# Kernel tuning notes

Measured on AMD Instinct MI355X. Metric: run time of the kernel, lower is better.

The kernel has to match this reference:

```python
import jax, jax.numpy as jnp
import numpy as np

TOPK = 2
GATE_THRESHOLD = 0.5
GATE_ALPHA = 0.1
EPS = 1e-8


def setup_inputs() -> dict:
    key = jax.random.key(0)
    x = jax.random.normal(key, (8192, 1024), dtype=jnp.float32)
    return {"x": x}


def reference(x):
    B, D = x.shape
    # F.normalize(p=2, eps): x / max(||x||, eps)
    norm = jnp.linalg.norm(x, axis=-1, keepdims=True)
    xn = x / jnp.maximum(norm, EPS)

    # pairwise dots; diagonal (self) masked to -1; NN search is no_grad
    dots = jax.lax.stop_gradient(xn @ xn.T)  # [B, B]
    diag = jnp.arange(B)
    dots = dots.at[diag, diag].set(-1.0)
    _, idx = jax.lax.top_k(dots, TOPK)  # [B, TOPK]

    nn_vecs = xn[idx]  # [B, TOPK, D]
    # torch PairwiseDistance(2, eps): ||x1 - x2 + eps||_2
    diff = xn[:, None, :] - nn_vecs + EPS
    distances = jnp.sqrt(jnp.sum(diff * diff, axis=-1)).reshape(-1)  # [B*TOPK]
    losses = -jnp.log(distances + EPS)

    # gate enabled since gate_threshold > 0
    alpha = max(GATE_ALPHA, 1e-6)
    gate = jax.nn.sigmoid((losses - GATE_THRESHOLD) / alpha)
    lg = losses * gate
    weighted_mean = lg.mean()
    gated_mean = lg.sum() / jnp.maximum(gate.sum(), 1.0)
    return 0.5 * weighted_mean + 0.5 * gated_mean
```

## Files before the change

### kernel.cpp

```cpp
#include <hip/hip_runtime.h>
#include <math.h>

#define NROWS 8192
#define DIM   1024
#define BT    256
#define NCHUNK 32
#define NTRI  528
#define NKT   16
#define BK    64

typedef __bf16 bf16x8 __attribute__((ext_vector_type(8)));
typedef float  f32x4  __attribute__((ext_vector_type(4)));

__device__ __forceinline__ unsigned short f2bf(float f) {
    unsigned int u = __float_as_uint(f);
    u = (u + 0x7FFFu + ((u >> 16) & 1u)) >> 16;
    return (unsigned short)u;
}

__device__ __forceinline__ void gld16(const void* g, void* l) {
    __builtin_amdgcn_global_load_lds(
        (__attribute__((address_space(1))) void*)g,
        (__attribute__((address_space(3))) void*)l,
        16, 0, 0);
}

template<int N>
__device__ __forceinline__ float dppror(float v) {
    return __int_as_float(__builtin_amdgcn_update_dpp(
        0, __float_as_int(v), 0x120 + N, 0xF, 0xF, false));
}

__device__ __forceinline__ void t2push(float& a1, float& a2, float v) {
    float hi = fmaxf(a1, v);
    float lo = fminf(a1, v);
    a1 = hi;
    a2 = fmaxf(a2, lo);
}

__device__ __forceinline__ void t2merge(float& a1, float& a2, float b1, float b2) {
    float hi = fmaxf(a1, b1);
    float lo = fminf(a1, b1);
    a1 = hi;
    a2 = fmaxf(fmaxf(a2, b2), lo);
}

__global__ __launch_bounds__(256) void knorm(const float* __restrict__ x,
                                             unsigned short* __restrict__ xn) {
    const int w = threadIdx.x >> 6, lane = threadIdx.x & 63;
    const int row = blockIdx.x * 4 + w;
    const float4* src = (const float4*)(x + (size_t)row * DIM);
    float4 v[4];
    float ss = 0.0f;
    #pragma unroll
    for (int i = 0; i < 4; i++) {
        v[i] = src[lane + 64 * i];
        ss += v[i].x * v[i].x + v[i].y * v[i].y + v[i].z * v[i].z + v[i].w * v[i].w;
    }
    #pragma unroll
    for (int d = 1; d < 64; d <<= 1) ss += __shfl_xor(ss, d);
    const float inv = 1.0f / fmaxf(sqrtf(ss), 1e-8f);
    unsigned short* dst = xn + (size_t)row * DIM;
    #pragma unroll
    for (int i = 0; i < 4; i++) {
        uint2 o;
        o.x = (unsigned)f2bf(v[i].x * inv) | ((unsigned)f2bf(v[i].y * inv) << 16);
        o.y = (unsigned)f2bf(v[i].z * inv) | ((unsigned)f2bf(v[i].w * inv) << 16);
        *(uint2*)(dst + (size_t)(lane + 64 * i) * 4) = o;
    }
}

__global__ __launch_bounds__(512, 2) void kgram(const unsigned short* __restrict__ xn,
                                                float2* __restrict__ top2) {
    __shared__ __align__(16) char smem[131072];
    float (*st2r)[256][2] = (float (*)[256][2])(smem);
    float (*st2c)[256][2] = (float (*)[256][2])(smem + 8192);

    const int t = threadIdx.x;
    const int lane = t & 63;
    const int w = t >> 6;
    const int wr = w >> 2, wc = w & 3;
    const int g = lane >> 4, c = lane & 15;
    const int cswz = (c >> 1) & 3;

    const int bid = (blockIdx.x & 7) * 66 + (blockIdx.x >> 3);
    int by = (int)((sqrtf(8.0f * (float)bid + 1.0f) - 1.0f) * 0.5f);
    while ((by + 1) * (by + 2) / 2 <= bid) by++;
    while (by * (by + 1) / 2 > bid) by--;
    const int bx = bid - by * (by + 1) / 2;
    const bool diagTile = (bx == by);

    const int q0 = t, q1 = 512 + t;
    const int r0 = q0 >> 2, c0 = (q0 & 3) ^ ((r0 >> 1) & 3);
    const int r1 = q1 >> 2, c1 = (q1 & 3) ^ ((r1 >> 1) & 3);
    const unsigned short* gA0p = xn + (size_t)(by * BT + r0) * DIM + c0 * 8;
    const unsigned short* gA1p = xn + (size_t)(by * BT + r1) * DIM + c1 * 8;
    const unsigned short* gB0p = xn + (size_t)(bx * BT + r0) * DIM + c0 * 8;
    const unsigned short* gB1p = xn + (size_t)(bx * BT + r1) * DIM + c1 * 8;

    const int aOff = (wr * 128 + c) * 64 + ((g ^ cswz) & 3) * 16;
    const int bOff = 65536 + (wc * 64 + c) * 64 + ((g ^ cswz) & 3) * 16;

    f32x4 acc[8][4];
    #pragma unroll
    for (int m = 0; m < 8; m++)
        #pragma unroll
        for (int n = 0; n < 4; n++) acc[m][n] = (f32x4)0.0f;

    bf16x8 aX0, aX1, aX2, aX3, aY0, aY1, aY2, aY3;
    bf16x8 bA0, bA1, bA2, bA3, bB0, bB1, bB2, bB3;

#define STG_A(BUF, H, KT) do {                                   \
        char* _d = smem + (BUF) * 32768 + (H) * 16384 + t * 16;  \
        gld16(gA0p + (KT) * 64 + (H) * 32, _d);                  \
        gld16(gA1p + (KT) * 64 + (H) * 32, _d + 8192);           \
    } while (0)
#define STG_B(BUF, H, KT) do {                                           \
        char* _d = smem + 65536 + (BUF) * 32768 + (H) * 16384 + t * 16;  \
        gld16(gB0p + (KT) * 64 + (H) * 32, _d);                          \
        gld16(gB1p + (KT) * 64 + (H) * 32, _d + 8192);                   \
    } while (0)
#define LDA4(D0, D1, D2, D3, BUF, H, MH) do {                                 \
        const char* _p = smem + (BUF) * 32768 + (H) * 16384 + (MH) * 4096 + aOff; \
        D0 = *(const bf16x8*)(_p);                                            \
        D1 = *(const bf16x8*)(_p + 1024);                                     \
        D2 = *(const bf16x8*)(_p + 2048);                                     \
        D3 = *(const bf16x8*)(_p + 3072);                                     \
    } while (0)
#define LDB4(D0, D1, D2, D3, BUF, H) do {                        \
        const char* _p = smem + (BUF) * 32768 + (H) * 16384 + bOff; \
        D0 = *(const bf16x8*)(_p);                               \
        D1 = *(const bf16x8*)(_p + 1024);                        \
        D2 = *(const bf16x8*)(_p + 2048);                        \
        D3 = *(const bf16x8*)(_p + 3072);                        \
    } while (0)
#define MF(a, b, cc) __builtin_amdgcn_mfma_f32_16x16x32_bf16(a, b, cc, 0, 0, 0)
#define MQUAD(MB, A0_, A1_, A2_, A3_, B0_, B1_, B2_, B3_) do {              \
        acc[(MB)+0][0]=MF(A0_,B0_,acc[(MB)+0][0]); acc[(MB)+0][1]=MF(A0_,B1_,acc[(MB)+0][1]); \
        acc[(MB)+0][2]=MF(A0_,B2_,acc[(MB)+0][2]); acc[(MB)+0][3]=MF(A0_,B3_,acc[(MB)+0][3]); \
        acc[(MB)+1][0]=MF(A1_,B0_,acc[(MB)+1][0]); acc[(MB)+1][1]=MF(A1_,B1_,acc[(MB)+1][1]); \
        acc[(MB)+1][2]=MF(A1_,B2_,acc[(MB)+1][2]); acc[(MB)+1][3]=MF(A1_,B3_,acc[(MB)+1][3]); \
        acc[(MB)+2][0]=MF(A2_,B0_,acc[(MB)+2][0]); acc[(MB)+2][1]=MF(A2_,B1_,acc[(MB)+2][1]); \
        acc[(MB)+2][2]=MF(A2_,B2_,acc[(MB)+2][2]); acc[(MB)+2][3]=MF(A2_,B3_,acc[(MB)+2][3]); \
        acc[(MB)+3][0]=MF(A3_,B0_,acc[(MB)+3][0]); acc[(MB)+3][1]=MF(A3_,B1_,acc[(MB)+3][1]); \
        acc[(MB)+3][2]=MF(A3_,B2_,acc[(MB)+3][2]); acc[(MB)+3][3]=MF(A3_,B3_,acc[(MB)+3][3]); \
    } while (0)
#define BAR1_LGKM                                          \
        __builtin_amdgcn_sched_barrier(0);                 \
        __builtin_amdgcn_s_barrier();                      \
        asm volatile("s_waitcnt lgkmcnt(0)" ::: "memory"); \
        __builtin_amdgcn_sched_barrier(0)
#define ENDPH                                              \
        __builtin_amdgcn_sched_barrier(0);                 \
        __builtin_amdgcn_s_barrier()
#define ENDPH_VM(N)                                        \
        __builtin_amdgcn_sched_barrier(0);                 \
        asm volatile("s_waitcnt vmcnt(" #N ")" ::: "memory"); \
        __builtin_amdgcn_s_barrier()

#define KTILE(J, BUF, S12, S34, VMA, VMB) do {                         \
                                                     \
        LDA4(aX0, aX1, aX2, aX3, BUF, 0, 0);                           \
        LDB4(bA0, bA1, bA2, bA3, BUF, 0);                              \
        if (S12) STG_A((BUF) ^ 1, 1, (J) + 1);                         \
        BAR1_LGKM;                                                     \
        __builtin_amdgcn_s_setprio(1);                                 \
        MQUAD(0, aX0, aX1, aX2, aX3, bA0, bA1, bA2, bA3);              \
        __builtin_amdgcn_s_setprio(0);                                 \
        ENDPH;                                                         \
                                                     \
        LDA4(aY0, aY1, aY2, aY3, BUF, 0, 1);                           \
        if (S12) STG_B((BUF) ^ 1, 1, (J) + 1);                         \
        BAR1_LGKM;                                                     \
        __builtin_amdgcn_s_setprio(1);                                 \
        MQUAD(4, aY0, aY1, aY2, aY3, bA0, bA1, bA2, bA3);              \
        __builtin_amdgcn_s_setprio(0);                                 \
        ENDPH_VM(VMA);                                                 \
                                                     \
        LDA4(aX0, aX1, aX2, aX3, BUF, 1, 0);                           \
        LDB4(bB0, bB1, bB2, bB3, BUF, 1);                              \
        if (S34) STG_A(BUF, 0, (J) + 2);                               \
        BAR1_LGKM;                                                     \
        __builtin_amdgcn_s_setprio(1);                                 \
        MQUAD(0, aX0, aX1, aX2, aX3, bB0, bB1, bB2, bB3);              \
        __builtin_amdgcn_s_setprio(0);                                 \
        ENDPH;                                                         \
                                                     \
        LDA4(aY0, aY1, aY2, aY3, BUF, 1, 1);                           \
        if (S34) STG_B(BUF, 0, (J) + 2);                               \
        BAR1_LGKM;                                                     \
        __builtin_amdgcn_s_setprio(1);                                 \
        MQUAD(4, aY0, aY1, aY2, aY3, bB0, bB1, bB2, bB3);              \
        __builtin_amdgcn_s_setprio(0);                                 \
        ENDPH_VM(VMB);                                                 \
    } while (0)

    STG_A(0, 0, 0); STG_B(0, 0, 0);
    STG_A(0, 1, 0); STG_B(0, 1, 0);
    STG_A(1, 0, 1); STG_B(1, 0, 1);
    __builtin_amdgcn_sched_barrier(0);
    asm volatile("s_waitcnt vmcnt(8)" ::: "memory");
    __builtin_amdgcn_s_barrier();
    __builtin_amdgcn_sched_barrier(0);

    #pragma unroll 1
    for (int jj = 0; jj < 7; ++jj) {
        const int j0 = jj * 2;
        KTILE(j0,     0, 1, 1, 8, 8);
        KTILE(j0 + 1, 1, 1, 1, 8, 8);
    }
    KTILE(14, 0, 1, 0, 8, 4);
    KTILE(15, 1, 0, 0, 0, 0);

#undef KTILE
#undef ENDPH_VM
#undef ENDPH
#undef BAR1_LGKM
#undef MQUAD
#undef MF
#undef LDB4
#undef LDA4
#undef STG_B
#undef STG_A

    #pragma unroll
    for (int m = 0; m < 8; m++) {
        #pragma unroll
        for (int rr = 0; rr < 4; rr++) {
            const int lrow = wr * 128 + m * 16 + g * 4 + rr;
            float a1 = -1e30f, a2 = -1e30f;
            #pragma unroll
            for (int n = 0; n < 4; n++) {
                float v = acc[m][n][rr];
                if (diagTile && (wc * 64 + n * 16 + c) == lrow) v = -2.0f;
                t2push(a1, a2, v);
            }
            { float b1 = dppror<1>(a1), b2 = dppror<1>(a2); t2merge(a1, a2, b1, b2); }
            { float b1 = dppror<2>(a1), b2 = dppror<2>(a2); t2merge(a1, a2, b1, b2); }
            { float b1 = dppror<4>(a1), b2 = dppror<4>(a2); t2merge(a1, a2, b1, b2); }
            { float b1 = dppror<8>(a1), b2 = dppror<8>(a2); t2merge(a1, a2, b1, b2); }
            if (c == 0) { st2r[wc][lrow][0] = a1; st2r[wc][lrow][1] = a2; }
        }
    }
    if (!diagTile) {
        #pragma unroll
        for (int n = 0; n < 4; n++) {
            const int lcol = wc * 64 + n * 16 + c;
            float a1 = -1e30f, a2 = -1e30f;
            #pragma unroll
            for (int m = 0; m < 8; m++)
                #pragma unroll
                for (int rr = 0; rr < 4; rr++)
                    t2push(a1, a2, acc[m][n][rr]);
            #pragma unroll
            for (int d = 16; d < 64; d <<= 1) {
                float b1 = __shfl_xor(a1, d);
                float b2 = __shfl_xor(a2, d);
                t2merge(a1, a2, b1, b2);
            }
            if (g == 0) { st2c[wr][lcol][0] = a1; st2c[wr][lcol][1] = a2; }
        }
    }
    __syncthreads();
    if (t < 256) {
        float a1 = st2r[0][t][0], a2 = st2r[0][t][1];
        t2merge(a1, a2, st2r[1][t][0], st2r[1][t][1]);
        t2merge(a1, a2, st2r[2][t][0], st2r[2][t][1]);
        t2merge(a1, a2, st2r[3][t][0], st2r[3][t][1]);
        top2[(size_t)(by * BT + t) * NCHUNK + bx] = make_float2(a1, a2);
    } else if (!diagTile) {
        const int tc = t - 256;
        float a1 = st2c[0][tc][0], a2 = st2c[0][tc][1];
        t2merge(a1, a2, st2c[1][tc][0], st2c[1][tc][1]);
        top2[(size_t)(bx * BT + tc) * NCHUNK + by] = make_float2(a1, a2);
    }
}

__global__ __launch_bounds__(256) void kloss(const float2* __restrict__ top2,
                                             float2* __restrict__ partials) {
    const int t = threadIdx.x;
    const int w = t >> 6, lane = t & 63;
    const int row = blockIdx.x * 4 + w;
    float a1 = -1e30f, a2 = -1e30f;
    if (lane < NCHUNK) {
        float2 q = top2[(size_t)row * NCHUNK + lane];
        a1 = q.x; a2 = q.y;
    }
    #pragma unroll
    for (int d = 1; d < 64; d <<= 1) {
        float b1 = __shfl_xor(a1, d);
        float b2 = __shfl_xor(a2, d);
        t2merge(a1, a2, b1, b2);
    }
    __shared__ float2 wsum[4];
    if (lane == 0) {
        float slg = 0.0f, sg = 0.0f;
        float vs[2] = {a1, a2};
        #pragma unroll
        for (int i = 0; i < 2; i++) {
            float dd = sqrtf(fmaxf(2.0f - 2.0f * vs[i], 0.0f));
            float loss = -logf(dd + 1e-8f);
            float gate = 1.0f / (1.0f + expf(-(loss - 0.5f) * 10.0f));
            slg += loss * gate;
            sg += gate;
        }
        wsum[w] = make_float2(slg, sg);
    }
    __syncthreads();
    if (t == 0) {
        float a = 0.0f, b = 0.0f;
        #pragma unroll
        for (int i = 0; i < 4; i++) { a += wsum[i].x; b += wsum[i].y; }
        partials[blockIdx.x] = make_float2(a, b);
    }
}

__global__ __launch_bounds__(256) void kfinal(const float2* __restrict__ partials,
                                              float* __restrict__ out) {
    const int t = threadIdx.x;
    float a = 0.0f, b = 0.0f;
    for (int i = t; i < 2048; i += 256) {
        float2 p = partials[i];
        a += p.x; b += p.y;
    }
    #pragma unroll
    for (int d = 1; d < 64; d <<= 1) {
        a += __shfl_xor(a, d);
        b += __shfl_xor(b, d);
    }
    __shared__ float2 ws4[4];
    if ((t & 63) == 0) ws4[t >> 6] = make_float2(a, b);
    __syncthreads();
    if (t == 0) {
        float A = 0.0f, Bb = 0.0f;
        #pragma unroll
        for (int i = 0; i < 4; i++) { A += ws4[i].x; Bb += ws4[i].y; }
        float wm = A / 16384.0f;
        float gm = A / fmaxf(Bb, 1.0f);
        out[0] = 0.5f * wm + 0.5f * gm;
    }
}

extern "C" void kernel_launch(void* const* d_in, const int* in_sizes, int n_in,
                              void* d_out, int out_size, void* d_ws, size_t ws_size,
                              hipStream_t stream) {
    const float* x = (const float*)d_in[0];
    unsigned short* xn = (unsigned short*)d_ws;
    float2* top2 = (float2*)((char*)d_ws + (size_t)16 * 1024 * 1024);
    float2* partials = (float2*)((char*)d_ws + (size_t)20 * 1024 * 1024);
    float* out = (float*)d_out;

    knorm<<<NROWS / 4, 256, 0, stream>>>(x, xn);
    kgram<<<NTRI, 512, 0, stream>>>(xn, top2);
    kloss<<<2048, 256, 0, stream>>>(top2, partials);
    kfinal<<<1, 256, 0, stream>>>(partials, out);
}
```

Baseline: 180.7 us.

## Split gram tiles into half-tile blocks with triple-buffered BK=32 pipeline and atomic final reduction

Each 256x256 upper-triangular tile is split into two 128x256 half-tiles. That gives 1056 blocks of 256 threads instead of 528 blocks of 512, which should balance work better across CUs. The K loop becomes a three-stage buffered pipeline with BK=32 over 32 steps. Column top-2 results are written straight to a 64-slot per-row table, and the separate final kernel is replaced by atomics plus a last-block-done counter in kloss. The cost is more redundant B-tile loads per block, more global writes, and float atomic ordering nondeterminism.

```diff
diff --git a/kernel.cpp b/kernel.cpp
--- a/kernel.cpp
+++ b/kernel.cpp
@@ -4,10 +4,11 @@
 #define NROWS 8192
 #define DIM   1024
 #define BT    256
-#define NCHUNK 32
+#define SLOTS 64
 #define NTRI  528
-#define NKT   16
-#define BK    64
+#define NBLK  1056
+#define NKT   32
+#define BK    32
 
 typedef __bf16 bf16x8 __attribute__((ext_vector_type(8)));
 typedef float  f32x4  __attribute__((ext_vector_type(4)));
@@ -46,7 +47,13 @@
 }
 
 __global__ __launch_bounds__(256) void knorm(const float* __restrict__ x,
-                                             unsigned short* __restrict__ xn) {
+                                             unsigned short* __restrict__ xn,
+                                             float* __restrict__ red) {
+    if (blockIdx.x == 0 && threadIdx.x == 0) {
+        red[0] = 0.0f;
+        red[1] = 0.0f;
+        ((unsigned int*)red)[2] = 0u;
+    }
     const int w = threadIdx.x >> 6, lane = threadIdx.x & 63;
     const int row = blockIdx.x * 4 + w;
     const float4* src = (const float4*)(x + (size_t)row * DIM);
@@ -70,36 +77,31 @@
     }
 }
 
-__global__ __launch_bounds__(512, 2) void kgram(const unsigned short* __restrict__ xn,
+__global__ __launch_bounds__(256, 2) void kgram(const unsigned short* __restrict__ xn,
                                                 float2* __restrict__ top2) {
-    __shared__ __align__(16) char smem[131072];
-    float (*st2r)[256][2] = (float (*)[256][2])(smem);
-    float (*st2c)[256][2] = (float (*)[256][2])(smem + 8192);
+    __shared__ __align__(16) char smem[73728];
+    float (*st2r)[128][2] = (float (*)[128][2])(smem);
 
     const int t = threadIdx.x;
     const int lane = t & 63;
     const int w = t >> 6;
-    const int wr = w >> 2, wc = w & 3;
     const int g = lane >> 4, c = lane & 15;
     const int cswz = (c >> 1) & 3;
 
-    const int bid = (blockIdx.x & 7) * 66 + (blockIdx.x >> 3);
-    int by = (int)((sqrtf(8.0f * (float)bid + 1.0f) - 1.0f) * 0.5f);
-    while ((by + 1) * (by + 2) / 2 <= bid) by++;
-    while (by * (by + 1) / 2 > bid) by--;
-    const int bx = bid - by * (by + 1) / 2;
+    const int bswz = (blockIdx.x & 7) * 132 + (blockIdx.x >> 3);
+    const int tix = bswz >> 1, hh = bswz & 1;
+    int by = (int)((sqrtf(8.0f * (float)tix + 1.0f) - 1.0f) * 0.5f);
+    while ((by + 1) * (by + 2) / 2 <= tix) by++;
+    while (by * (by + 1) / 2 > tix) by--;
+    const int bx = tix - by * (by + 1) / 2;
     const bool diagTile = (bx == by);
 
-    const int q0 = t, q1 = 512 + t;
-    const int r0 = q0 >> 2, c0 = (q0 & 3) ^ ((r0 >> 1) & 3);
-    const int r1 = q1 >> 2, c1 = (q1 & 3) ^ ((r1 >> 1) & 3);
-    const unsigned short* gA0p = xn + (size_t)(by * BT + r0) * DIM + c0 * 8;
-    const unsigned short* gA1p = xn + (size_t)(by * BT + r1) * DIM + c1 * 8;
+    const int r0 = t >> 2;
+    const int c0 = (t & 3) ^ ((r0 >> 1) & 3);
+    const unsigned short* gA0p = xn + (size_t)(by * BT + hh * 128 + r0) * DIM + c0 * 8;
     const unsigned short* gB0p = xn + (size_t)(bx * BT + r0) * DIM + c0 * 8;
-    const unsigned short* gB1p = xn + (size_t)(bx * BT + r1) * DIM + c1 * 8;
-
-    const int aOff = (wr * 128 + c) * 64 + ((g ^ cswz) & 3) * 16;
-    const int bOff = 65536 + (wc * 64 + c) * 64 + ((g ^ cswz) & 3) * 16;
+
+    const int aBase = c * 64 + ((g ^ cswz) & 3) * 16;
 
     f32x4 acc[8][4];
     #pragma unroll
@@ -107,43 +109,46 @@
         #pragma unroll
         for (int n = 0; n < 4; n++) acc[m][n] = (f32x4)0.0f;
 
-    bf16x8 aX0, aX1, aX2, aX3, aY0, aY1, aY2, aY3;
-    bf16x8 bA0, bA1, bA2, bA3, bB0, bB1, bB2, bB3;
-
-#define STG_A(BUF, H, KT) do {                                   \
-        char* _d = smem + (BUF) * 32768 + (H) * 16384 + t * 16;  \
-        gld16(gA0p + (KT) * 64 + (H) * 32, _d);                  \
-        gld16(gA1p + (KT) * 64 + (H) * 32, _d + 8192);           \
-    } while (0)
-#define STG_B(BUF, H, KT) do {                                           \
-        char* _d = smem + 65536 + (BUF) * 32768 + (H) * 16384 + t * 16;  \
-        gld16(gB0p + (KT) * 64 + (H) * 32, _d);                          \
-        gld16(gB1p + (KT) * 64 + (H) * 32, _d + 8192);                   \
-    } while (0)
-#define LDA4(D0, D1, D2, D3, BUF, H, MH) do {                                 \
-        const char* _p = smem + (BUF) * 32768 + (H) * 16384 + (MH) * 4096 + aOff; \
-        D0 = *(const bf16x8*)(_p);                                            \
-        D1 = *(const bf16x8*)(_p + 1024);                                     \
-        D2 = *(const bf16x8*)(_p + 2048);                                     \
-        D3 = *(const bf16x8*)(_p + 3072);                                     \
-    } while (0)
-#define LDB4(D0, D1, D2, D3, BUF, H) do {                        \
-        const char* _p = smem + (BUF) * 32768 + (H) * 16384 + bOff; \
-        D0 = *(const bf16x8*)(_p);                               \
-        D1 = *(const bf16x8*)(_p + 1024);                        \
-        D2 = *(const bf16x8*)(_p + 2048);                        \
-        D3 = *(const bf16x8*)(_p + 3072);                        \
+    bf16x8 aX0, aX1, aX2, aX3, aY0, aY1, aY2, aY3, bX0, bX1, bX2, bX3;
+
+#define STG_A(BUF, KT) do {                                  \
+        char* _d = smem + (BUF) * 24576 + t * 16;            \
+        const unsigned short* _s = gA0p + (KT) * BK;         \
+        gld16(_s, _d);                                       \
+        gld16(_s + 65536, _d + 4096);                        \
+    } while (0)
+#define STG_B(BUF, KT) do {                                  \
+        char* _d = smem + (BUF) * 24576 + 8192 + t * 16;     \
+        const unsigned short* _s = gB0p + (KT) * BK;         \
+        gld16(_s, _d);                                       \
+        gld16(_s + 65536,  _d + 4096);                       \
+        gld16(_s + 131072, _d + 8192);                       \
+        gld16(_s + 196608, _d + 12288);                      \
+    } while (0)
+#define LDA4(D0, D1, D2, D3, BUF, MH) do {                              \
+        const char* _p = smem + (BUF) * 24576 + (MH) * 4096 + aBase;    \
+        D0 = *(const bf16x8*)(_p);                                      \
+        D1 = *(const bf16x8*)(_p + 1024);                               \
+        D2 = *(const bf16x8*)(_p + 2048);                               \
+        D3 = *(const bf16x8*)(_p + 3072);                               \
+    } while (0)
+#define LDB4(D0, D1, D2, D3, BUF) do {                                  \
+        const char* _p = smem + (BUF) * 24576 + 8192 + w * 4096 + aBase; \
+        D0 = *(const bf16x8*)(_p);                                      \
+        D1 = *(const bf16x8*)(_p + 1024);                               \
+        D2 = *(const bf16x8*)(_p + 2048);                               \
+        D3 = *(const bf16x8*)(_p + 3072);                               \
     } while (0)
 #define MF(a, b, cc) __builtin_amdgcn_mfma_f32_16x16x32_bf16(a, b, cc, 0, 0, 0)
-#define MQUAD(MB, A0_, A1_, A2_, A3_, B0_, B1_, B2_, B3_) do {              \
-        acc[(MB)+0][0]=MF(A0_,B0_,acc[(MB)+0][0]); acc[(MB)+0][1]=MF(A0_,B1_,acc[(MB)+0][1]); \
-        acc[(MB)+0][2]=MF(A0_,B2_,acc[(MB)+0][2]); acc[(MB)+0][3]=MF(A0_,B3_,acc[(MB)+0][3]); \
-        acc[(MB)+1][0]=MF(A1_,B0_,acc[(MB)+1][0]); acc[(MB)+1][1]=MF(A1_,B1_,acc[(MB)+1][1]); \
-        acc[(MB)+1][2]=MF(A1_,B2_,acc[(MB)+1][2]); acc[(MB)+1][3]=MF(A1_,B3_,acc[(MB)+1][3]); \
-        acc[(MB)+2][0]=MF(A2_,B0_,acc[(MB)+2][0]); acc[(MB)+2][1]=MF(A2_,B1_,acc[(MB)+2][1]); \
-        acc[(MB)+2][2]=MF(A2_,B2_,acc[(MB)+2][2]); acc[(MB)+2][3]=MF(A2_,B3_,acc[(MB)+2][3]); \
-        acc[(MB)+3][0]=MF(A3_,B0_,acc[(MB)+3][0]); acc[(MB)+3][1]=MF(A3_,B1_,acc[(MB)+3][1]); \
-        acc[(MB)+3][2]=MF(A3_,B2_,acc[(MB)+3][2]); acc[(MB)+3][3]=MF(A3_,B3_,acc[(MB)+3][3]); \
+#define MQUAD(MB, A0_, A1_, A2_, A3_) do {                                                    \
+        acc[(MB)+0][0]=MF(A0_,bX0,acc[(MB)+0][0]); acc[(MB)+0][1]=MF(A0_,bX1,acc[(MB)+0][1]); \
+        acc[(MB)+0][2]=MF(A0_,bX2,acc[(MB)+0][2]); acc[(MB)+0][3]=MF(A0_,bX3,acc[(MB)+0][3]); \
+        acc[(MB)+1][0]=MF(A1_,bX0,acc[(MB)+1][0]); acc[(MB)+1][1]=MF(A1_,bX1,acc[(MB)+1][1]); \
+        acc[(MB)+1][2]=MF(A1_,bX2,acc[(MB)+1][2]); acc[(MB)+1][3]=MF(A1_,bX3,acc[(MB)+1][3]); \
+        acc[(MB)+2][0]=MF(A2_,bX0,acc[(MB)+2][0]); acc[(MB)+2][1]=MF(A2_,bX1,acc[(MB)+2][1]); \
+        acc[(MB)+2][2]=MF(A2_,bX2,acc[(MB)+2][2]); acc[(MB)+2][3]=MF(A2_,bX3,acc[(MB)+2][3]); \
+        acc[(MB)+3][0]=MF(A3_,bX0,acc[(MB)+3][0]); acc[(MB)+3][1]=MF(A3_,bX1,acc[(MB)+3][1]); \
+        acc[(MB)+3][2]=MF(A3_,bX2,acc[(MB)+3][2]); acc[(MB)+3][3]=MF(A3_,bX3,acc[(MB)+3][3]); \
     } while (0)
 #define BAR1_LGKM                                          \
         __builtin_amdgcn_sched_barrier(0);                 \
@@ -158,61 +163,42 @@
         asm volatile("s_waitcnt vmcnt(" #N ")" ::: "memory"); \
         __builtin_amdgcn_s_barrier()
 
-#define KTILE(J, BUF, S12, S34, VMA, VMB) do {                         \
-                                                     \
-        LDA4(aX0, aX1, aX2, aX3, BUF, 0, 0);                           \
-        LDB4(bA0, bA1, bA2, bA3, BUF, 0);                              \
-        if (S12) STG_A((BUF) ^ 1, 1, (J) + 1);                         \
-        BAR1_LGKM;                                                     \
-        __builtin_amdgcn_s_setprio(1);                                 \
-        MQUAD(0, aX0, aX1, aX2, aX3, bA0, bA1, bA2, bA3);              \
-        __builtin_amdgcn_s_setprio(0);                                 \
-        ENDPH;                                                         \
-                                                     \
-        LDA4(aY0, aY1, aY2, aY3, BUF, 0, 1);                           \
-        if (S12) STG_B((BUF) ^ 1, 1, (J) + 1);                         \
-        BAR1_LGKM;                                                     \
-        __builtin_amdgcn_s_setprio(1);                                 \
-        MQUAD(4, aY0, aY1, aY2, aY3, bA0, bA1, bA2, bA3);              \
-        __builtin_amdgcn_s_setprio(0);                                 \
-        ENDPH_VM(VMA);                                                 \
-                                                     \
-        LDA4(aX0, aX1, aX2, aX3, BUF, 1, 0);                           \
-        LDB4(bB0, bB1, bB2, bB3, BUF, 1);                              \
-        if (S34) STG_A(BUF, 0, (J) + 2);                               \
-        BAR1_LGKM;                                                     \
-        __builtin_amdgcn_s_setprio(1);                                 \
-        MQUAD(0, aX0, aX1, aX2, aX3, bB0, bB1, bB2, bB3);              \
-        __builtin_amdgcn_s_setprio(0);                                 \
-        ENDPH;                                                         \
-                                                     \
-        LDA4(aY0, aY1, aY2, aY3, BUF, 1, 1);                           \
-        if (S34) STG_B(BUF, 0, (J) + 2);                               \
-        BAR1_LGKM;                                                     \
-        __builtin_amdgcn_s_setprio(1);                                 \
-        MQUAD(4, aY0, aY1, aY2, aY3, bB0, bB1, bB2, bB3);              \
-        __builtin_amdgcn_s_setprio(0);                                 \
-        ENDPH_VM(VMB);                                                 \
-    } while (0)
-
-    STG_A(0, 0, 0); STG_B(0, 0, 0);
-    STG_A(0, 1, 0); STG_B(0, 1, 0);
-    STG_A(1, 0, 1); STG_B(1, 0, 1);
+#define KSTEP(J, BUF, SBUF, DOSTG, ENDM)            \
+    do {                                            \
+        LDA4(aX0, aX1, aX2, aX3, BUF, 0);           \
+        LDB4(bX0, bX1, bX2, bX3, BUF);              \
+        if (DOSTG) STG_A(SBUF, (J) + 2);            \
+        BAR1_LGKM;                                  \
+        __builtin_amdgcn_s_setprio(1);              \
+        MQUAD(0, aX0, aX1, aX2, aX3);               \
+        __builtin_amdgcn_s_setprio(0);              \
+        ENDPH;                                      \
+        LDA4(aY0, aY1, aY2, aY3, BUF, 1);           \
+        if (DOSTG) STG_B(SBUF, (J) + 2);            \
+        BAR1_LGKM;                                  \
+        __builtin_amdgcn_s_setprio(1);              \
+        MQUAD(4, aY0, aY1, aY2, aY3);               \
+        __builtin_amdgcn_s_setprio(0);              \
+        ENDM;                                       \
+    } while (0)
+
+    STG_A(0, 0); STG_B(0, 0);
+    STG_A(1, 1); STG_B(1, 1);
     __builtin_amdgcn_sched_barrier(0);
-    asm volatile("s_waitcnt vmcnt(8)" ::: "memory");
+    asm volatile("s_waitcnt vmcnt(6)" ::: "memory");
     __builtin_amdgcn_s_barrier();
     __builtin_amdgcn_sched_barrier(0);
 
     #pragma unroll 1
-    for (int jj = 0; jj < 7; ++jj) {
-        const int j0 = jj * 2;
-        KTILE(j0,     0, 1, 1, 8, 8);
-        KTILE(j0 + 1, 1, 1, 1, 8, 8);
-    }
-    KTILE(14, 0, 1, 0, 8, 4);
-    KTILE(15, 1, 0, 0, 0, 0);
-
-#undef KTILE
+    for (int jj = 0; jj < 10; ++jj) {
+        KSTEP(3 * jj + 0, 0, 2, 1, ENDPH_VM(6));
+        KSTEP(3 * jj + 1, 1, 0, 1, ENDPH_VM(6));
+        KSTEP(3 * jj + 2, 2, 1, 1, ENDPH_VM(6));
+    }
+    KSTEP(30, 0, 0, 0, ENDPH_VM(0));
+    KSTEP(31, 1, 0, 0, (void)0);
+
+#undef KSTEP
 #undef ENDPH_VM
 #undef ENDPH
 #undef BAR1_LGKM
@@ -227,25 +213,24 @@
     for (int m = 0; m < 8; m++) {
         #pragma unroll
         for (int rr = 0; rr < 4; rr++) {
-            const int lrow = wr * 128 + m * 16 + g * 4 + rr;
+            const int lrow = m * 16 + g * 4 + rr;
             float a1 = -1e30f, a2 = -1e30f;
             #pragma unroll
             for (int n = 0; n < 4; n++) {
                 float v = acc[m][n][rr];
-                if (diagTile && (wc * 64 + n * 16 + c) == lrow) v = -2.0f;
+                if (diagTile && (w * 64 + n * 16 + c) == hh * 128 + lrow) v = -2.0f;
                 t2push(a1, a2, v);
             }
             { float b1 = dppror<1>(a1), b2 = dppror<1>(a2); t2merge(a1, a2, b1, b2); }
             { float b1 = dppror<2>(a1), b2 = dppror<2>(a2); t2merge(a1, a2, b1, b2); }
             { float b1 = dppror<4>(a1), b2 = dppror<4>(a2); t2merge(a1, a2, b1, b2); }
             { float b1 = dppror<8>(a1), b2 = dppror<8>(a2); t2merge(a1, a2, b1, b2); }
-            if (c == 0) { st2r[wc][lrow][0] = a1; st2r[wc][lrow][1] = a2; }
+            if (c == 0) { st2r[w][lrow][0] = a1; st2r[w][lrow][1] = a2; }
         }
     }
     if (!diagTile) {
         #pragma unroll
         for (int n = 0; n < 4; n++) {
-            const int lcol = wc * 64 + n * 16 + c;
             float a1 = -1e30f, a2 = -1e30f;
             #pragma unroll
             for (int m = 0; m < 8; m++)
@@ -258,32 +243,32 @@
                 float b2 = __shfl_xor(a2, d);
                 t2merge(a1, a2, b1, b2);
             }
-            if (g == 0) { st2c[wr][lcol][0] = a1; st2c[wr][lcol][1] = a2; }
+            if (g == 0)
+                top2[(size_t)(bx * BT + w * 64 + n * 16 + c) * SLOTS + 2 * by + hh] =
+                    make_float2(a1, a2);
         }
     }
     __syncthreads();
-    if (t < 256) {
+    if (t < 128) {
         float a1 = st2r[0][t][0], a2 = st2r[0][t][1];
         t2merge(a1, a2, st2r[1][t][0], st2r[1][t][1]);
         t2merge(a1, a2, st2r[2][t][0], st2r[2][t][1]);
         t2merge(a1, a2, st2r[3][t][0], st2r[3][t][1]);
-        top2[(size_t)(by * BT + t) * NCHUNK + bx] = make_float2(a1, a2);
-    } else if (!diagTile) {
-        const int tc = t - 256;
-        float a1 = st2c[0][tc][0], a2 = st2c[0][tc][1];
-        t2merge(a1, a2, st2c[1][tc][0], st2c[1][tc][1]);
-        top2[(size_t)(bx * BT + tc) * NCHUNK + by] = make_float2(a1, a2);
+        top2[(size_t)(by * BT + hh * 128 + t) * SLOTS + 2 * bx] = make_float2(a1, a2);
     }
 }
 
 __global__ __launch_bounds__(256) void kloss(const float2* __restrict__ top2,
-                                             float2* __restrict__ partials) {
+                                             float* __restrict__ red,
+                                             float* __restrict__ out) {
     const int t = threadIdx.x;
     const int w = t >> 6, lane = t & 63;
     const int row = blockIdx.x * 4 + w;
+    const int cr = row >> 8;
+    const bool valid = !((lane & 1) && ((lane >> 1) <= cr));
     float a1 = -1e30f, a2 = -1e30f;
-    if (lane < NCHUNK) {
-        float2 q = top2[(size_t)row * NCHUNK + lane];
+    if (valid) {
+        float2 q = top2[(size_t)row * SLOTS + lane];
         a1 = q.x; a2 = q.y;
     }
     #pragma unroll
@@ -308,36 +293,19 @@
     }
     __syncthreads();
     if (t == 0) {
-        float a = 0.0f, b = 0.0f;
-        #pragma unroll
-        for (int i = 0; i < 4; i++) { a += wsum[i].x; b += wsum[i].y; }
-        partials[blockIdx.x] = make_float2(a, b);
-    }
-}
-
-__global__ __launch_bounds__(256) void kfinal(const float2* __restrict__ partials,
-                                              float* __restrict__ out) {
-    const int t = threadIdx.x;
-    float a = 0.0f, b = 0.0f;
-    for (int i = t; i < 2048; i += 256) {
-        float2 p = partials[i];
-        a += p.x; b += p.y;
-    }
-    #pragma unroll
-    for (int d = 1; d < 64; d <<= 1) {
-        a += __shfl_xor(a, d);
-        b += __shfl_xor(b, d);
-    }
-    __shared__ float2 ws4[4];
-    if ((t & 63) == 0) ws4[t >> 6] = make_float2(a, b);
-    __syncthreads();
-    if (t == 0) {
-        float A = 0.0f, Bb = 0.0f;
-        #pragma unroll
-        for (int i = 0; i < 4; i++) { A += ws4[i].x; Bb += ws4[i].y; }
-        float wm = A / 16384.0f;
-        float gm = A / fmaxf(Bb, 1.0f);
-        out[0] = 0.5f * wm + 0.5f * gm;
+        float a = wsum[0].x + wsum[1].x + wsum[2].x + wsum[3].x;
+        float b = wsum[0].y + wsum[1].y + wsum[2].y + wsum[3].y;
+        atomicAdd(&red[0], a);
+        atomicAdd(&red[1], b);
+        __threadfence();
+        unsigned int old = atomicAdd((unsigned int*)red + 2, 1u);
+        if (old == 2047u) {
+            float A  = atomicAdd(&red[0], 0.0f);
+            float Bb = atomicAdd(&red[1], 0.0f);
+            float wm = A / 16384.0f;
+            float gm = A / fmaxf(Bb, 1.0f);
+            out[0] = 0.5f * wm + 0.5f * gm;
+        }
     }
 }
 
@@ -347,11 +315,10 @@
     const float* x = (const float*)d_in[0];
     unsigned short* xn = (unsigned short*)d_ws;
     float2* top2 = (float2*)((char*)d_ws + (size_t)16 * 1024 * 1024);
-    float2* partials = (float2*)((char*)d_ws + (size_t)20 * 1024 * 1024);
+    float* red = (float*)((char*)d_ws + (size_t)20 * 1024 * 1024);
     float* out = (float*)d_out;
 
-    knorm<<<NROWS / 4, 256, 0, stream>>>(x, xn);
-    kgram<<<NTRI, 512, 0, stream>>>(xn, top2);
-    kloss<<<2048, 256, 0, stream>>>(top2, partials);
-    kfinal<<<1, 256, 0, stream>>>(partials, out);
-}
+    knorm<<<NROWS / 4, 256, 0, stream>>>(x, xn, red);
+    kgram<<<NBLK, 256, 0, stream>>>(xn, top2);
+    kloss<<<2048, 256, 0, stream>>>(top2, red, out);
+}
```

Result: slower. 237.2 us (+31.3%).
